# Kernel tuning notes

Measured on AMD Instinct MI355X. Metric: run time of the kernel, lower is better.

The kernel has to match this reference:

```python
import jax, jax.numpy as jnp
import numpy as np
from math import factorial
from functools import lru_cache

LMAX1, LMAX2, N = 3, 3, 500000


def _cg_su2(j1, m1, j2, m2, j3, m3):
    # Standard Clebsch-Gordan coefficient <j1 m1 j2 m2 | j3 m3> (Racah formula)
    if m3 != m1 + m2:
        return 0.0
    f = factorial
    pref = ((2 * j3 + 1) * f(j3 + j1 - j2) * f(j3 - j1 + j2) * f(j1 + j2 - j3) / f(j1 + j2 + j3 + 1)) ** 0.5
    pref *= (f(j3 + m3) * f(j3 - m3) * f(j1 - m1) * f(j1 + m1) * f(j2 - m2) * f(j2 + m2)) ** 0.5
    s = 0.0
    for k in range(0, j1 + j2 - j3 + 1):
        if min(j1 - m1 - k, j2 + m2 - k, j3 - j2 + m1 + k, j3 - j1 - m2 + k) < 0:
            continue
        s += (-1) ** k / (f(k) * f(j1 + j2 - j3 - k) * f(j1 - m1 - k) * f(j2 + m2 - k) * f(j3 - j2 + m1 + k) * f(j3 - j1 - m2 + k))
    return pref * s


def _real_to_complex(l):
    # change of basis real SH -> complex SH, with (-i)^l phase so CG tensor is real
    q = np.zeros((2 * l + 1, 2 * l + 1), dtype=complex)
    for m in range(-l, 0):
        q[l + m, l - m] = 2 ** -0.5
        q[l + m, l + m] = -1j * 2 ** -0.5
    q[l, l] = 1.0
    for m in range(1, l + 1):
        q[l + m, l + m] = (-1) ** m * 2 ** -0.5
        q[l + m, l - m] = 1j * (-1) ** m * 2 ** -0.5
    return (-1j) ** l * q


@lru_cache(maxsize=None)
def CG_SO3(l1, l2, l3):
    # Real-basis Wigner-3j-like tensor, Frobenius-normalized to 1 (3j normalization)
    C = np.zeros((2 * l1 + 1, 2 * l2 + 1, 2 * l3 + 1))
    for m1 in range(-l1, l1 + 1):
        for m2 in range(-l2, l2 + 1):
            m3 = m1 + m2
            if abs(m3) <= l3:
                C[l1 + m1, l2 + m2, l3 + m3] = _cg_su2(l1, m1, l2, m2, l3, m3)
    Q1, Q2, Q3 = _real_to_complex(l1), _real_to_complex(l2), _real_to_complex(l3)
    Cr = np.real(np.einsum('ij,kl,mn,ikm->jln', Q1, Q2, np.conj(Q3), C.astype(complex)))
    return Cr / np.linalg.norm(Cr)


@lru_cache(maxsize=None)
def build_w3j(lmax1, lmax2, lmax_out=None, ignore_parity=False):
    irreps_1 = [(l, (-1) ** l) for l in range(lmax1 + 1)]
    irreps_2 = [(l, (-1) ** l) for l in range(lmax2 + 1)]
    lsout, psout, i12 = [], [], []
    lmax_o = lmax_out if lmax_out is not None else lmax1 + lmax2
    for i1, (l1, p1) in enumerate(irreps_1):
        for i2, (l2, p2) in enumerate(irreps_2):
            for lout in range(abs(l1 - l2), l1 + l2 + 1):
                if p1 * p2 != (-1) ** lout and not ignore_parity:
                    continue
                if lout > lmax_o:
                    continue
                lsout.append(lout); psout.append(p1 * p2); i12.append((i1, i2))
    lsout = np.array(lsout); psout = np.array(psout)
    idx = np.lexsort((psout, lsout))
    lsout, psout = lsout[idx], psout[idx]
    i12 = [i12[i] for i in idx]
    irreps_out = [(int(l), int(p)) for l, p in zip(lsout, psout)]
    s1 = np.concatenate([[0], np.cumsum([2 * l + 1 for l, _ in irreps_1])])
    s2 = np.concatenate([[0], np.cumsum([2 * l + 1 for l, _ in irreps_2])])
    so = np.concatenate([[0], np.cumsum([2 * l + 1 for l, _ in irreps_out])])
    w3js = np.zeros(((lmax1 + 1) ** 2, (lmax2 + 1) ** 2, int(so[-1])), dtype=np.float32)
    for iout, (lout, pout) in enumerate(irreps_out):
        i1, i2 = i12[iout]
        l1, l2 = irreps_1[i1][0], irreps_2[i2][0]
        w3js[s1[i1]:s1[i1 + 1], s2[i2]:s2[i2 + 1], so[iout]:so[iout + 1]] = CG_SO3(l1, l2, lout) * (2 * lout + 1) ** 0.5
    return jnp.asarray(w3js)


def setup_inputs() -> dict:
    key = jax.random.key(0)
    k1, k2 = jax.random.split(key)
    d1, d2 = (LMAX1 + 1) ** 2, (LMAX2 + 1) ** 2
    x1 = jax.random.normal(k1, (N, d1), dtype=jnp.float32)
    x2 = jax.random.normal(k2, (N, d2), dtype=jnp.float32)
    return {"x1": x1, "x2": x2}


def reference(x1, x2):
    w3j = build_w3j(LMAX1, LMAX2)  # [16, 16, 170] block-sparse CG tensor
    return jnp.einsum('...a,...b,abc->...c', x1, x2, w3j)
```

## Files before the change

kernel.cpp:

```cpp
#include <hip/hip_runtime.h>
#include <stdint.h>


struct PathT { int l1, l2, l3, so; };

__constant__ PathT g_paths[30] = {
    {0,0,0,0},{1,1,0,1},{2,2,0,2},{3,3,0,3},
    {0,1,1,4},{1,0,1,7},{1,2,1,10},{2,1,1,13},{2,3,1,16},{3,2,1,19},
    {0,2,2,22},{1,1,2,27},{1,3,2,32},{2,0,2,37},{2,2,2,42},{3,1,2,47},{3,3,2,52},
    {0,3,3,57},{1,2,3,64},{2,1,3,71},{2,3,3,78},{3,0,3,85},{3,2,3,92},
    {1,3,4,99},{2,2,4,108},{3,1,4,117},{3,3,4,126},
    {2,3,5,135},{3,2,5,146},
    {3,3,6,157}
};

__constant__ int g_off[30] = {
    0,1,10,35, 84,93,102,147,192,297, 402,427,472,577,602,727,832,
    1077,1126,1231,1336,1581,1630, 1875,2064,2289,2478, 2919,3304, 3689
};

static constexpr int P_L1[30] = {0,1,2,3, 0,1,1,2,2,3, 0,1,1,2,2,3,3, 0,1,2,2,3,3, 1,2,3,3, 2,3, 3};
static constexpr int P_L2[30] = {0,1,2,3, 1,0,2,1,3,2, 2,1,3,0,2,1,3, 3,2,1,3,0,2, 3,2,1,3, 3,2, 3};
static constexpr int P_L3[30] = {0,0,0,0, 1,1,1,1,1,1, 2,2,2,2,2,2,2, 3,3,3,3,3,3, 4,4,4,4, 5,5, 6};

__constant__ double g_fact[14] = {
    1.0, 1.0, 2.0, 6.0, 24.0, 120.0, 720.0, 5040.0, 40320.0, 362880.0,
    3628800.0, 39916800.0, 479001600.0, 6227020800.0
};

struct cd { double re, im; };

__device__ __forceinline__ cd cmul(cd a, cd b) {
    return { a.re*b.re - a.im*b.im, a.re*b.im + a.im*b.re };
}

__device__ double cg_su2(int j1, int m1, int j2, int m2, int j3, int m3) {
    if (m3 != m1 + m2) return 0.0;
    double pref = sqrt((double)(2*j3+1) * g_fact[j3+j1-j2] * g_fact[j3-j1+j2]
                       * g_fact[j1+j2-j3] / g_fact[j1+j2+j3+1]);
    pref *= sqrt(g_fact[j3+m3]*g_fact[j3-m3]*g_fact[j1-m1]*g_fact[j1+m1]
                 *g_fact[j2-m2]*g_fact[j2+m2]);
    double s = 0.0;
    for (int k = 0; k <= j1+j2-j3; ++k) {
        int a = j1-m1-k, b = j2+m2-k, c = j3-j2+m1+k, d = j3-j1-m2+k;
        if (a < 0 || b < 0 || c < 0 || d < 0) continue;
        double t = 1.0 / (g_fact[k]*g_fact[j1+j2-j3-k]*g_fact[a]*g_fact[b]
                          *g_fact[c]*g_fact[d]);
        s += (k & 1) ? -t : t;
    }
    return pref * s;
}

__device__ cd qent(int l, int row, int col) {
    const double is2 = 0.70710678118654752440;
    int m = row - l;
    cd q = {0.0, 0.0};
    if (m < 0) {
        if (col == l - m)      q = { is2, 0.0 };
        else if (col == l + m) q = { 0.0, -is2 };
    } else if (m == 0) {
        if (col == l)          q = { 1.0, 0.0 };
    } else {
        double sgn = (m & 1) ? -1.0 : 1.0;
        if (col == l + m)      q = { sgn*is2, 0.0 };
        else if (col == l - m) q = { 0.0, sgn*is2 };
    }
    switch (l & 3) {
        case 1: q = {  q.im, -q.re }; break;
        case 2: q = { -q.re, -q.im }; break;
        case 3: q = { -q.im,  q.re }; break;
        default: break;
    }
    return q;
}

__global__ void detect_dtype_kernel(const unsigned short* __restrict__ x,
                                    int n_u16_min, int* __restrict__ flag) {
    __shared__ int s[256];
    const int tid = threadIdx.x;
    int ncheck = n_u16_min < 8192 ? n_u16_min : 8192;
    int good = 0;
    for (int i = tid; i < ncheck; i += 256) {
        unsigned short v = x[i];
        int e = (v >> 7) & 0xFF;
        good += (v == 0 || (e >= 97 && e <= 158)) ? 1 : 0;
    }
    s[tid] = good;
    __syncthreads();
    for (int t = 128; t > 0; t >>= 1) {
        if (tid < t) s[tid] += s[tid + t];
        __syncthreads();
    }
    if (tid == 0) *flag = (s[0] * 10 >= ncheck * 9) ? 1 : 0;
}

__global__ void build_w3j_kernel(float* __restrict__ dense) {
    const int p  = blockIdx.x;
    const int l1 = g_paths[p].l1, l2 = g_paths[p].l2, l3 = g_paths[p].l3;
    const int so = g_paths[p].so;
    const int D1 = 2*l1+1, D2 = 2*l2+1, D3 = 2*l3+1;
    const int M  = D1*D2*D3;
    const int tid = threadIdx.x;

    __shared__ double sC[49];
    __shared__ double sCr[640];
    __shared__ double sred[256];

    for (int e = tid; e < D1*D2; e += blockDim.x) {
        int i = e / D2, k = e - i*D2;
        int m1 = i - l1, m2 = k - l2, m3 = m1 + m2;
        int am3 = m3 < 0 ? -m3 : m3;
        sC[e] = (am3 <= l3) ? cg_su2(l1, m1, l2, m2, l3, m3) : 0.0;
    }
    __syncthreads();

    double part = 0.0;
    for (int e = tid; e < M; e += blockDim.x) {
        int j  = e / (D2*D3);
        int r  = e - j*(D2*D3);
        int li = r / D3;
        int n  = r - li*D3;
        cd z = {0.0, 0.0};
        for (int i = 0; i < D1; ++i) {
            for (int k = 0; k < D2; ++k) {
                int m3 = (i - l1) + (k - l2);
                if (m3 < -l3 || m3 > l3) continue;
                double cval = sC[i*D2 + k];
                if (cval == 0.0) continue;
                cd q1 = qent(l1, i, j);
                if (q1.re == 0.0 && q1.im == 0.0) continue;
                cd q2 = qent(l2, k, li);
                if (q2.re == 0.0 && q2.im == 0.0) continue;
                cd q3 = qent(l3, l3 + m3, n);
                q3.im = -q3.im;
                cd t = cmul(cmul(q1, q2), q3);
                z.re += t.re * cval;
                z.im += t.im * cval;
            }
        }
        sCr[e] = z.re;
        part += z.re * z.re;
    }
    sred[tid] = part;
    __syncthreads();
    for (int s = 128; s > 0; s >>= 1) {
        if (tid < s) sred[tid] += sred[tid + s];
        __syncthreads();
    }
    const double scale = sqrt((double)(2*l3+1)) / sqrt(sred[0]);

    for (int e = tid; e < M; e += blockDim.x) {
        int j  = e / (D2*D3);
        int r  = e - j*(D2*D3);
        int li = r / D3;
        int n  = r - li*D3;
        int a = l1*l1 + j, b = l2*l2 + li, c = so + n;
        dense[(a*16 + b)*170 + c] = (float)(sCr[e] * scale);
    }
}

__global__ void repack_kernel(const float* __restrict__ dense,
                              float* __restrict__ Cpk) {
    const int p  = blockIdx.x;
    const int l1 = g_paths[p].l1, l2 = g_paths[p].l2, l3 = g_paths[p].l3;
    const int so = g_paths[p].so;
    const int D1 = 2*l1+1, D2 = 2*l2+1, D3 = 2*l3+1;
    const int M  = D1*D2*D3;
    const int base = g_off[p];
    for (int e = threadIdx.x; e < M; e += blockDim.x) {
        int mo = e / (D1*D2);
        int r  = e - mo*(D1*D2);
        int m1 = r / D2;
        int m2 = r - m1*D2;
        int a = l1*l1 + m1, b = l2*l2 + m2, c = so + mo;
        Cpk[base + e] = dense[(a*16 + b)*170 + c];
    }
}

__device__ __forceinline__ unsigned bf16_rne(float x) {
    unsigned xb = __float_as_uint(x);
    return (xb + 0x7fffu + ((xb >> 16) & 1u)) >> 16;
}

template<int MODE>
__device__ __forceinline__ void tp_row_body(const void* __restrict__ x1v,
                                            const void* __restrict__ x2v,
                                            const float* __restrict__ Cpk,
                                            void* __restrict__ outv,
                                            int row) {
    float X1[16], X2[16];

    if (MODE) {
        const unsigned short* p1 = (const unsigned short*)x1v + (long)row*16;
        const unsigned short* p2 = (const unsigned short*)x2v + (long)row*16;
        uint4 a0 = *reinterpret_cast<const uint4*>(p1);
        uint4 a1 = *reinterpret_cast<const uint4*>(p1 + 8);
        uint4 b0 = *reinterpret_cast<const uint4*>(p2);
        uint4 b1 = *reinterpret_cast<const uint4*>(p2 + 8);
        unsigned wa[8] = {a0.x,a0.y,a0.z,a0.w,a1.x,a1.y,a1.z,a1.w};
        unsigned wb[8] = {b0.x,b0.y,b0.z,b0.w,b1.x,b1.y,b1.z,b1.w};
        #pragma unroll
        for (int i = 0; i < 8; ++i) {
            X1[2*i]   = __uint_as_float(wa[i] << 16);
            X1[2*i+1] = __uint_as_float(wa[i] & 0xFFFF0000u);
            X2[2*i]   = __uint_as_float(wb[i] << 16);
            X2[2*i+1] = __uint_as_float(wb[i] & 0xFFFF0000u);
        }
    } else {
        const float4* f1 = reinterpret_cast<const float4*>((const float*)x1v + (long)row*16);
        const float4* f2 = reinterpret_cast<const float4*>((const float*)x2v + (long)row*16);
        #pragma unroll
        for (int q = 0; q < 4; ++q) {
            float4 v1 = f1[q], v2 = f2[q];
            X1[q*4+0] = v1.x; X1[q*4+1] = v1.y; X1[q*4+2] = v1.z; X1[q*4+3] = v1.w;
            X2[q*4+0] = v2.x; X2[q*4+1] = v2.y; X2[q*4+2] = v2.z; X2[q*4+3] = v2.w;
        }
    }

    float pend = 0.0f;
    int c   = 0;
    int off = 0;

    #pragma unroll
    for (int p = 0; p < 30; ++p) {
        const int l1 = P_L1[p], l2 = P_L2[p], l3 = P_L3[p];
        const int D1 = 2*l1+1, D2 = 2*l2+1, D3 = 2*l3+1;

        #pragma unroll
        for (int mo = 0; mo < D3; ++mo) {
            const int mu3 = (mo < l3) ? (l3 - mo) : (mo - l3);
            float acc = 0.0f;
            #pragma unroll
            for (int m1 = 0; m1 < D1; ++m1) {
                const int mu1 = (m1 < l1) ? (l1 - m1) : (m1 - l1);
                float partial = 0.0f;
                int used = 0;
                #pragma unroll
                for (int m2 = 0; m2 < D2; ++m2) {
                    const int mu2 = (m2 < l2) ? (l2 - m2) : (m2 - l2);
                    const int dmu = (mu1 > mu2) ? (mu1 - mu2) : (mu2 - mu1);
                    if (mu3 == mu1 + mu2 || mu3 == dmu) {
                        partial = fmaf(Cpk[off + (mo*D1 + m1)*D2 + m2],
                                       X2[l2*l2 + m2], partial);
                        used = 1;
                    }
                }
                if (used) acc = fmaf(X1[l1*l1 + m1], partial, acc);
            }

            if (c & 1) {
                if (MODE) {
                    unsigned u = bf16_rne(pend) | (bf16_rne(acc) << 16);
                    *reinterpret_cast<unsigned*>(
                        (unsigned short*)outv + (long)row*170 + (c - 1)) = u;
                } else {
                    *reinterpret_cast<float2*>(
                        (float*)outv + (long)row*170 + (c - 1)) =
                        make_float2(pend, acc);
                }
            } else {
                pend = acc;
            }
            ++c;
        }
        off += D1*D2*D3;
    }
}

__global__ __launch_bounds__(256)
void tp_dense_kernel(const void* __restrict__ x1v,
                     const void* __restrict__ x2v,
                     const float* __restrict__ Cpk,
                     const int*  __restrict__ flag,
                     void* __restrict__ outv,
                     int nrows) {
    const int row = blockIdx.x * blockDim.x + threadIdx.x;
    if (row >= nrows) return;
    if (*flag) tp_row_body<1>(x1v, x2v, Cpk, outv, row);
    else       tp_row_body<0>(x1v, x2v, Cpk, outv, row);
}

extern "C" void kernel_launch(void* const* d_in, const int* in_sizes, int n_in,
                              void* d_out, int out_size, void* d_ws, size_t ws_size,
                              hipStream_t stream) {
    const void* x1 = d_in[0];
    const void* x2 = d_in[1];

    char*  ws    = (char*)d_ws;
    float* dense = (float*)ws;
    float* Cpk   = (float*)(ws + 174080);
    int*   flag  = (int*)(ws + 245824);

    int nrows = in_sizes[0] / 16;

    detect_dtype_kernel<<<dim3(1), dim3(256), 0, stream>>>(
        (const unsigned short*)x1, in_sizes[0], flag);
    build_w3j_kernel<<<dim3(30), dim3(256), 0, stream>>>(dense);
    repack_kernel<<<dim3(30), dim3(256), 0, stream>>>(dense, Cpk);

    int nblocks = (nrows + 255) / 256;
    tp_dense_kernel<<<dim3(nblocks), dim3(256), 0, stream>>>(
        x1, x2, Cpk, flag, d_out, nrows);
}
```

Baseline: 572.2 us.

## Bake CG coefficients at compile time and stage output through LDS for coalesced stores

The Clebsch-Gordan coefficients are now computed with constexpr functions and folded into the kernel as immediates. This removes the two setup kernels and the coefficient loads, and lets the compiler skip zero coefficients. Output rows are staged per wavefront in shared memory in 16-column chunks, then written cooperatively so that neighbouring lanes store contiguous 16-byte segments instead of strided per-row float2 writes. This adds LDS traffic and raises register pressure from inlined constants in exchange for fewer launches and better-coalesced global stores.

Measured after the change: 481.7 us. -15.8%, faster.

```diff
diff --git a/kernel.cpp b/kernel.cpp
--- a/kernel.cpp
+++ b/kernel.cpp
@@ -2,59 +2,56 @@
 #include <stdint.h>
 
 
-struct PathT { int l1, l2, l3, so; };
-
-__constant__ PathT g_paths[30] = {
-    {0,0,0,0},{1,1,0,1},{2,2,0,2},{3,3,0,3},
-    {0,1,1,4},{1,0,1,7},{1,2,1,10},{2,1,1,13},{2,3,1,16},{3,2,1,19},
-    {0,2,2,22},{1,1,2,27},{1,3,2,32},{2,0,2,37},{2,2,2,42},{3,1,2,47},{3,3,2,52},
-    {0,3,3,57},{1,2,3,64},{2,1,3,71},{2,3,3,78},{3,0,3,85},{3,2,3,92},
-    {1,3,4,99},{2,2,4,108},{3,1,4,117},{3,3,4,126},
-    {2,3,5,135},{3,2,5,146},
-    {3,3,6,157}
-};
-
-__constant__ int g_off[30] = {
-    0,1,10,35, 84,93,102,147,192,297, 402,427,472,577,602,727,832,
-    1077,1126,1231,1336,1581,1630, 1875,2064,2289,2478, 2919,3304, 3689
-};
-
-static constexpr int P_L1[30] = {0,1,2,3, 0,1,1,2,2,3, 0,1,1,2,2,3,3, 0,1,2,2,3,3, 1,2,3,3, 2,3, 3};
-static constexpr int P_L2[30] = {0,1,2,3, 1,0,2,1,3,2, 2,1,3,0,2,1,3, 3,2,1,3,0,2, 3,2,1,3, 3,2, 3};
-static constexpr int P_L3[30] = {0,0,0,0, 1,1,1,1,1,1, 2,2,2,2,2,2,2, 3,3,3,3,3,3, 4,4,4,4, 5,5, 6};
-
-__constant__ double g_fact[14] = {
+constexpr int PL1c[30] = {0,1,2,3, 0,1,1,2,2,3, 0,1,1,2,2,3,3, 0,1,2,2,3,3, 1,2,3,3, 2,3, 3};
+constexpr int PL2c[30] = {0,1,2,3, 1,0,2,1,3,2, 2,1,3,0,2,1,3, 3,2,1,3,0,2, 3,2,1,3, 3,2, 3};
+constexpr int PL3c[30] = {0,0,0,0, 1,1,1,1,1,1, 2,2,2,2,2,2,2, 3,3,3,3,3,3, 4,4,4,4, 5,5, 6};
+constexpr int SOc[30]  = {0,1,2,3, 4,7,10,13,16,19, 22,27,32,37,42,47,52,
+                          57,64,71,78,85,92, 99,108,117,126, 135,146, 157};
+constexpr int OFFc[30] = {0,1,10,35, 84,93,102,147,192,297, 402,427,472,577,602,727,832,
+                          1077,1126,1231,1336,1581,1630, 1875,2064,2289,2478, 2919,3304, 3689};
+
+
+constexpr double FACT[14] = {
     1.0, 1.0, 2.0, 6.0, 24.0, 120.0, 720.0, 5040.0, 40320.0, 362880.0,
     3628800.0, 39916800.0, 479001600.0, 6227020800.0
 };
 
-struct cd { double re, im; };
-
-__device__ __forceinline__ cd cmul(cd a, cd b) {
+constexpr double csqrt(double x) {
+    if (x <= 0.0) return 0.0;
+    double y = 1.0;
+    for (int i = 0; i < 600 && y * y < x; ++i)       y *= 2.0;
+    for (int i = 0; i < 600 && y * y > 4.0 * x; ++i) y *= 0.5;
+    for (int i = 0; i < 8; ++i) y = 0.5 * (y + x / y);
+    return y;
+}
+
+struct CDc { double re, im; };
+
+constexpr CDc cmulc(CDc a, CDc b) {
     return { a.re*b.re - a.im*b.im, a.re*b.im + a.im*b.re };
 }
 
-__device__ double cg_su2(int j1, int m1, int j2, int m2, int j3, int m3) {
+constexpr double cg_su2_c(int j1, int m1, int j2, int m2, int j3, int m3) {
     if (m3 != m1 + m2) return 0.0;
-    double pref = sqrt((double)(2*j3+1) * g_fact[j3+j1-j2] * g_fact[j3-j1+j2]
-                       * g_fact[j1+j2-j3] / g_fact[j1+j2+j3+1]);
-    pref *= sqrt(g_fact[j3+m3]*g_fact[j3-m3]*g_fact[j1-m1]*g_fact[j1+m1]
-                 *g_fact[j2-m2]*g_fact[j2+m2]);
+    double pref = csqrt((double)(2*j3+1) * FACT[j3+j1-j2] * FACT[j3-j1+j2]
+                        * FACT[j1+j2-j3] / FACT[j1+j2+j3+1]);
+    pref *= csqrt(FACT[j3+m3]*FACT[j3-m3]*FACT[j1-m1]*FACT[j1+m1]
+                  *FACT[j2-m2]*FACT[j2+m2]);
     double s = 0.0;
     for (int k = 0; k <= j1+j2-j3; ++k) {
         int a = j1-m1-k, b = j2+m2-k, c = j3-j2+m1+k, d = j3-j1-m2+k;
         if (a < 0 || b < 0 || c < 0 || d < 0) continue;
-        double t = 1.0 / (g_fact[k]*g_fact[j1+j2-j3-k]*g_fact[a]*g_fact[b]
-                          *g_fact[c]*g_fact[d]);
+        double t = 1.0 / (FACT[k]*FACT[j1+j2-j3-k]*FACT[a]*FACT[b]
+                          *FACT[c]*FACT[d]);
         s += (k & 1) ? -t : t;
     }
     return pref * s;
 }
 
-__device__ cd qent(int l, int row, int col) {
+constexpr CDc qent_c(int l, int row, int col) {
     const double is2 = 0.70710678118654752440;
     int m = row - l;
-    cd q = {0.0, 0.0};
+    CDc q = {0.0, 0.0};
     if (m < 0) {
         if (col == l - m)      q = { is2, 0.0 };
         else if (col == l + m) q = { 0.0, -is2 };
@@ -73,6 +70,97 @@
     }
     return q;
 }
+
+struct PathDat { float coef[637]; };
+
+template<int P>
+constexpr PathDat build_path() {
+    const int l1 = PL1c[P], l2 = PL2c[P], l3 = PL3c[P];
+    const int D1 = 2*l1+1, D2 = 2*l2+1, D3 = 2*l3+1;
+    double cg[7][7] = {};
+    for (int i = 0; i < D1; ++i)
+        for (int k = 0; k < D2; ++k) {
+            int m1 = i - l1, m2 = k - l2, m3 = m1 + m2;
+            cg[i][k] = (m3 >= -l3 && m3 <= l3) ? cg_su2_c(l1,m1,l2,m2,l3,m3) : 0.0;
+        }
+    double vals[637] = {};
+    double nrm = 0.0;
+    for (int mo = 0; mo < D3; ++mo) {
+        int mu3 = mo < l3 ? l3 - mo : mo - l3;
+        for (int j = 0; j < D1; ++j) {
+            int mu1 = j < l1 ? l1 - j : j - l1;
+            for (int li = 0; li < D2; ++li) {
+                int mu2 = li < l2 ? l2 - li : li - l2;
+                int dmu = mu1 > mu2 ? mu1 - mu2 : mu2 - mu1;
+                if (!(mu3 == mu1 + mu2 || mu3 == dmu)) continue;
+                double val = 0.0;
+                for (int s1 = 0; s1 < 2; ++s1) {
+                    int i = s1 ? 2*l1 - j : j;
+                    if (s1 && i == j) break;
+                    CDc q1 = qent_c(l1, i, j);
+                    if (q1.re == 0.0 && q1.im == 0.0) continue;
+                    for (int s2 = 0; s2 < 2; ++s2) {
+                        int k = s2 ? 2*l2 - li : li;
+                        if (s2 && k == li) break;
+                        int m3 = (i - l1) + (k - l2);
+                        if (m3 < -l3 || m3 > l3) continue;
+                        double cval = cg[i][k];
+                        if (cval == 0.0) continue;
+                        CDc q2 = qent_c(l2, k, li);
+                        if (q2.re == 0.0 && q2.im == 0.0) continue;
+                        CDc q3 = qent_c(l3, l3 + m3, mo);
+                        q3.im = -q3.im;
+                        CDc t = cmulc(cmulc(q1, q2), q3);
+                        val += t.re * cval;
+                    }
+                }
+                vals[(mo*D1 + j)*D2 + li] = val;
+                nrm += val * val;
+            }
+        }
+    }
+    double scale = csqrt((double)(2*l3+1)) / csqrt(nrm);
+    PathDat t{};
+    for (int e = 0; e < D1*D2*D3; ++e) t.coef[e] = (float)(vals[e] * scale);
+    return t;
+}
+
+constexpr PathDat PD00 = build_path<0>();  constexpr PathDat PD01 = build_path<1>();
+constexpr PathDat PD02 = build_path<2>();  constexpr PathDat PD03 = build_path<3>();
+constexpr PathDat PD04 = build_path<4>();  constexpr PathDat PD05 = build_path<5>();
+constexpr PathDat PD06 = build_path<6>();  constexpr PathDat PD07 = build_path<7>();
+constexpr PathDat PD08 = build_path<8>();  constexpr PathDat PD09 = build_path<9>();
+constexpr PathDat PD10 = build_path<10>(); constexpr PathDat PD11 = build_path<11>();
+constexpr PathDat PD12 = build_path<12>(); constexpr PathDat PD13 = build_path<13>();
+constexpr PathDat PD14 = build_path<14>(); constexpr PathDat PD15 = build_path<15>();
+constexpr PathDat PD16 = build_path<16>(); constexpr PathDat PD17 = build_path<17>();
+constexpr PathDat PD18 = build_path<18>(); constexpr PathDat PD19 = build_path<19>();
+constexpr PathDat PD20 = build_path<20>(); constexpr PathDat PD21 = build_path<21>();
+constexpr PathDat PD22 = build_path<22>(); constexpr PathDat PD23 = build_path<23>();
+constexpr PathDat PD24 = build_path<24>(); constexpr PathDat PD25 = build_path<25>();
+constexpr PathDat PD26 = build_path<26>(); constexpr PathDat PD27 = build_path<27>();
+constexpr PathDat PD28 = build_path<28>(); constexpr PathDat PD29 = build_path<29>();
+
+struct Flat { float c[4326]; };
+
+constexpr Flat merge_all() {
+    const PathDat* t[30] = {
+        &PD00,&PD01,&PD02,&PD03,&PD04,&PD05,&PD06,&PD07,&PD08,&PD09,
+        &PD10,&PD11,&PD12,&PD13,&PD14,&PD15,&PD16,&PD17,&PD18,&PD19,
+        &PD20,&PD21,&PD22,&PD23,&PD24,&PD25,&PD26,&PD27,&PD28,&PD29
+    };
+    Flat f{};
+    int o = 0;
+    for (int p = 0; p < 30; ++p) {
+        int M = (2*PL1c[p]+1) * (2*PL2c[p]+1) * (2*PL3c[p]+1);
+        for (int e = 0; e < M; ++e) f.c[o + e] = t[p]->coef[e];
+        o += M;
+    }
+    return f;
+}
+
+constexpr Flat FT = merge_all();
+
 
 __global__ void detect_dtype_kernel(const unsigned short* __restrict__ x,
                                     int n_u16_min, int* __restrict__ flag) {
@@ -94,105 +182,74 @@
     if (tid == 0) *flag = (s[0] * 10 >= ncheck * 9) ? 1 : 0;
 }
 
-__global__ void build_w3j_kernel(float* __restrict__ dense) {
-    const int p  = blockIdx.x;
-    const int l1 = g_paths[p].l1, l2 = g_paths[p].l2, l3 = g_paths[p].l3;
-    const int so = g_paths[p].so;
-    const int D1 = 2*l1+1, D2 = 2*l2+1, D3 = 2*l3+1;
-    const int M  = D1*D2*D3;
-    const int tid = threadIdx.x;
-
-    __shared__ double sC[49];
-    __shared__ double sCr[640];
-    __shared__ double sred[256];
-
-    for (int e = tid; e < D1*D2; e += blockDim.x) {
-        int i = e / D2, k = e - i*D2;
-        int m1 = i - l1, m2 = k - l2, m3 = m1 + m2;
-        int am3 = m3 < 0 ? -m3 : m3;
-        sC[e] = (am3 <= l3) ? cg_su2(l1, m1, l2, m2, l3, m3) : 0.0;
-    }
-    __syncthreads();
-
-    double part = 0.0;
-    for (int e = tid; e < M; e += blockDim.x) {
-        int j  = e / (D2*D3);
-        int r  = e - j*(D2*D3);
-        int li = r / D3;
-        int n  = r - li*D3;
-        cd z = {0.0, 0.0};
-        for (int i = 0; i < D1; ++i) {
-            for (int k = 0; k < D2; ++k) {
-                int m3 = (i - l1) + (k - l2);
-                if (m3 < -l3 || m3 > l3) continue;
-                double cval = sC[i*D2 + k];
-                if (cval == 0.0) continue;
-                cd q1 = qent(l1, i, j);
-                if (q1.re == 0.0 && q1.im == 0.0) continue;
-                cd q2 = qent(l2, k, li);
-                if (q2.re == 0.0 && q2.im == 0.0) continue;
-                cd q3 = qent(l3, l3 + m3, n);
-                q3.im = -q3.im;
-                cd t = cmul(cmul(q1, q2), q3);
-                z.re += t.re * cval;
-                z.im += t.im * cval;
-            }
-        }
-        sCr[e] = z.re;
-        part += z.re * z.re;
-    }
-    sred[tid] = part;
-    __syncthreads();
-    for (int s = 128; s > 0; s >>= 1) {
-        if (tid < s) sred[tid] += sred[tid + s];
-        __syncthreads();
-    }
-    const double scale = sqrt((double)(2*l3+1)) / sqrt(sred[0]);
-
-    for (int e = tid; e < M; e += blockDim.x) {
-        int j  = e / (D2*D3);
-        int r  = e - j*(D2*D3);
-        int li = r / D3;
-        int n  = r - li*D3;
-        int a = l1*l1 + j, b = l2*l2 + li, c = so + n;
-        dense[(a*16 + b)*170 + c] = (float)(sCr[e] * scale);
-    }
-}
-
-__global__ void repack_kernel(const float* __restrict__ dense,
-                              float* __restrict__ Cpk) {
-    const int p  = blockIdx.x;
-    const int l1 = g_paths[p].l1, l2 = g_paths[p].l2, l3 = g_paths[p].l3;
-    const int so = g_paths[p].so;
-    const int D1 = 2*l1+1, D2 = 2*l2+1, D3 = 2*l3+1;
-    const int M  = D1*D2*D3;
-    const int base = g_off[p];
-    for (int e = threadIdx.x; e < M; e += blockDim.x) {
-        int mo = e / (D1*D2);
-        int r  = e - mo*(D1*D2);
-        int m1 = r / D2;
-        int m2 = r - m1*D2;
-        int a = l1*l1 + m1, b = l2*l2 + m2, c = so + mo;
-        Cpk[base + e] = dense[(a*16 + b)*170 + c];
-    }
-}
-
 __device__ __forceinline__ unsigned bf16_rne(float x) {
     unsigned xb = __float_as_uint(x);
     return (xb + 0x7fffu + ((xb >> 16) & 1u)) >> 16;
 }
 
+struct alignas(8) F4 { float x, y, z, w; };
+
+template<int MODE>
+__device__ __forceinline__ void flush_chunk(float (&tile)[64][18], int lane,
+                                            long rowbase, int c0,
+                                            void* __restrict__ outv, int nrows) {
+    const int r0 = lane >> 2, p = lane & 3;
+    #pragma unroll
+    for (int g = 0; g < 4; ++g) {
+        const int rr = r0 + g * 16;
+        const long grow = rowbase + rr;
+        if (grow < nrows) {
+            const float* s = &tile[rr][p * 4];
+            float v0 = s[0], v1 = s[1], v2 = s[2], v3 = s[3];
+            if (MODE) {
+                unsigned* dst = (unsigned*)((unsigned short*)outv
+                                            + grow * 170 + c0 + p * 4);
+                dst[0] = bf16_rne(v0) | (bf16_rne(v1) << 16);
+                dst[1] = bf16_rne(v2) | (bf16_rne(v3) << 16);
+            } else {
+                F4* dst = (F4*)((float*)outv + grow * 170 + c0 + p * 4);
+                *dst = F4{v0, v1, v2, v3};
+            }
+        }
+    }
+}
+
+template<int MODE>
+__device__ __forceinline__ void flush_tail(float (&tile)[64][18], int lane,
+                                           long rowbase,
+                                           void* __restrict__ outv, int nrows) {
+    const long grow = rowbase + lane;
+    if (grow >= nrows) return;
+    if (MODE) {
+        unsigned short* orow = (unsigned short*)outv + grow * 170 + 160;
+        #pragma unroll
+        for (int j = 0; j < 5; ++j) {
+            unsigned u = bf16_rne(tile[lane][2*j])
+                       | (bf16_rne(tile[lane][2*j + 1]) << 16);
+            *(unsigned*)(orow + 2*j) = u;
+        }
+    } else {
+        float* orow = (float*)outv + grow * 170 + 160;
+        #pragma unroll
+        for (int j = 0; j < 5; ++j)
+            *(float2*)(orow + 2*j) = make_float2(tile[lane][2*j],
+                                                 tile[lane][2*j + 1]);
+    }
+}
+
 template<int MODE>
 __device__ __forceinline__ void tp_row_body(const void* __restrict__ x1v,
                                             const void* __restrict__ x2v,
-                                            const float* __restrict__ Cpk,
                                             void* __restrict__ outv,
-                                            int row) {
+                                            float (&tile)[64][18],
+                                            int lane, long rowbase, int nrows) {
+    const long row = rowbase + lane;
+    const long rc  = row < nrows ? row : (long)nrows - 1;
+
     float X1[16], X2[16];
-
     if (MODE) {
-        const unsigned short* p1 = (const unsigned short*)x1v + (long)row*16;
-        const unsigned short* p2 = (const unsigned short*)x2v + (long)row*16;
+        const unsigned short* p1 = (const unsigned short*)x1v + rc * 16;
+        const unsigned short* p2 = (const unsigned short*)x2v + rc * 16;
         uint4 a0 = *reinterpret_cast<const uint4*>(p1);
         uint4 a1 = *reinterpret_cast<const uint4*>(p1 + 8);
         uint4 b0 = *reinterpret_cast<const uint4*>(p2);
@@ -207,8 +264,8 @@
             X2[2*i+1] = __uint_as_float(wb[i] & 0xFFFF0000u);
         }
     } else {
-        const float4* f1 = reinterpret_cast<const float4*>((const float*)x1v + (long)row*16);
-        const float4* f2 = reinterpret_cast<const float4*>((const float*)x2v + (long)row*16);
+        const float4* f1 = reinterpret_cast<const float4*>((const float*)x1v + rc * 16);
+        const float4* f2 = reinterpret_cast<const float4*>((const float*)x2v + rc * 16);
         #pragma unroll
         for (int q = 0; q < 4; ++q) {
             float4 v1 = f1[q], v2 = f2[q];
@@ -218,66 +275,62 @@
     }
 
     float pend = 0.0f;
-    int c   = 0;
-    int off = 0;
 
     #pragma unroll
     for (int p = 0; p < 30; ++p) {
-        const int l1 = P_L1[p], l2 = P_L2[p], l3 = P_L3[p];
+        const int l1 = PL1c[p], l2 = PL2c[p], l3 = PL3c[p];
         const int D1 = 2*l1+1, D2 = 2*l2+1, D3 = 2*l3+1;
+        const int off = OFFc[p];
 
         #pragma unroll
         for (int mo = 0; mo < D3; ++mo) {
+            const int c   = SOc[p] + mo;
             const int mu3 = (mo < l3) ? (l3 - mo) : (mo - l3);
             float acc = 0.0f;
             #pragma unroll
             for (int m1 = 0; m1 < D1; ++m1) {
                 const int mu1 = (m1 < l1) ? (l1 - m1) : (m1 - l1);
                 float partial = 0.0f;
-                int used = 0;
+                bool used = false;
                 #pragma unroll
                 for (int m2 = 0; m2 < D2; ++m2) {
                     const int mu2 = (m2 < l2) ? (l2 - m2) : (m2 - l2);
                     const int dmu = (mu1 > mu2) ? (mu1 - mu2) : (mu2 - mu1);
                     if (mu3 == mu1 + mu2 || mu3 == dmu) {
-                        partial = fmaf(Cpk[off + (mo*D1 + m1)*D2 + m2],
-                                       X2[l2*l2 + m2], partial);
-                        used = 1;
+                        const float cf = FT.c[off + (mo*D1 + m1)*D2 + m2];
+                        if (cf != 0.0f) {
+                            partial = fmaf(cf, X2[l2*l2 + m2], partial);
+                            used = true;
+                        }
                     }
                 }
                 if (used) acc = fmaf(X1[l1*l1 + m1], partial, acc);
             }
 
             if (c & 1) {
-                if (MODE) {
-                    unsigned u = bf16_rne(pend) | (bf16_rne(acc) << 16);
-                    *reinterpret_cast<unsigned*>(
-                        (unsigned short*)outv + (long)row*170 + (c - 1)) = u;
-                } else {
-                    *reinterpret_cast<float2*>(
-                        (float*)outv + (long)row*170 + (c - 1)) =
-                        make_float2(pend, acc);
-                }
+                *(float2*)&tile[lane][(c - 1) & 15] = make_float2(pend, acc);
+                if ((c & 15) == 15)
+                    flush_chunk<MODE>(tile, lane, rowbase, c & ~15, outv, nrows);
             } else {
                 pend = acc;
             }
-            ++c;
-        }
-        off += D1*D2*D3;
-    }
+        }
+    }
+    flush_tail<MODE>(tile, lane, rowbase, outv, nrows);
 }
 
 __global__ __launch_bounds__(256)
 void tp_dense_kernel(const void* __restrict__ x1v,
                      const void* __restrict__ x2v,
-                     const float* __restrict__ Cpk,
                      const int*  __restrict__ flag,
                      void* __restrict__ outv,
                      int nrows) {
-    const int row = blockIdx.x * blockDim.x + threadIdx.x;
-    if (row >= nrows) return;
-    if (*flag) tp_row_body<1>(x1v, x2v, Cpk, outv, row);
-    else       tp_row_body<0>(x1v, x2v, Cpk, outv, row);
+    __shared__ float stage[4][64][18];
+    const int w    = threadIdx.x >> 6;
+    const int lane = threadIdx.x & 63;
+    const long rowbase = (long)blockIdx.x * 256 + w * 64;
+    if (*flag) tp_row_body<1>(x1v, x2v, outv, stage[w], lane, rowbase, nrows);
+    else       tp_row_body<0>(x1v, x2v, outv, stage[w], lane, rowbase, nrows);
 }
 
 extern "C" void kernel_launch(void* const* d_in, const int* in_sizes, int n_in,
@@ -286,19 +339,14 @@
     const void* x1 = d_in[0];
     const void* x2 = d_in[1];
 
-    char*  ws    = (char*)d_ws;
-    float* dense = (float*)ws;
-    float* Cpk   = (float*)(ws + 174080);
-    int*   flag  = (int*)(ws + 245824);
+    int* flag = (int*)d_ws;
 
     int nrows = in_sizes[0] / 16;
 
     detect_dtype_kernel<<<dim3(1), dim3(256), 0, stream>>>(
         (const unsigned short*)x1, in_sizes[0], flag);
-    build_w3j_kernel<<<dim3(30), dim3(256), 0, stream>>>(dense);
-    repack_kernel<<<dim3(30), dim3(256), 0, stream>>>(dense, Cpk);
 
     int nblocks = (nrows + 255) / 256;
     tp_dense_kernel<<<dim3(nblocks), dim3(256), 0, stream>>>(
-        x1, x2, Cpk, flag, d_out, nrows);
-}
+        x1, x2, flag, d_out, nrows);
+}
```
